# Optimization experiments

Hardware: AMD Instinct MI355X
Metric: run time of the kernel (lower is better)

Reference implementation:

```python
import jax, jax.numpy as jnp
import numpy as np

VOCAB = 256
D_MODEL = 1792
NUM_LAYERS = 4
D_STATE = 16
D_CONV = 4
EXPAND = 2
D_INNER = EXPAND * D_MODEL            # 3584
DT_RANK = (D_MODEL + 15) // 16        # 112
EPS = 1e-5


def _ln(x, w, b):
    x32 = x.astype(jnp.float32)
    mu = x32.mean(-1, keepdims=True)
    var = ((x32 - mu) ** 2).mean(-1, keepdims=True)
    return (((x32 - mu) * jax.lax.rsqrt(var + EPS)) * w + b)


def _silu(x):
    return x * jax.nn.sigmoid(x)


def _mamba_mixer(x, in_w, cw, cb, xp_w, dt_w, dt_b, A_log, Dp, out_w):
    # x: [B, L, d_model]
    B, L, _ = x.shape
    xz = jnp.einsum('bld,ed->ble', x, in_w)          # [B, L, 2*d_inner]
    xc, z = jnp.split(xz, 2, axis=-1)
    # depthwise causal conv1d over time
    xc = jax.lax.conv_general_dilated(
        xc.swapaxes(1, 2), cw[:, None, :], (1,), [(D_CONV - 1, 0)],
        feature_group_count=D_INNER,
        dimension_numbers=('NCH', 'OIH', 'NCH')).swapaxes(1, 2) + cb
    xc = _silu(xc)
    dbl = jnp.einsum('bld,ed->ble', xc, xp_w)        # [B, L, dt_rank+2*d_state]
    dt = dbl[..., :DT_RANK]
    Bm = dbl[..., DT_RANK:DT_RANK + D_STATE]
    Cm = dbl[..., DT_RANK + D_STATE:]
    dt = jax.nn.softplus(jnp.einsum('blr,dr->bld', dt, dt_w) + dt_b)  # [B,L,d_inner]
    A = -jnp.exp(A_log)                              # [d_inner, d_state]
    dA = jnp.exp(dt[..., None] * A)                  # [B, L, d_inner, d_state]
    dBx = dt[..., None] * Bm[:, :, None, :] * xc[..., None]

    def step(h, t):
        dA_t, dBx_t, C_t = t
        h = dA_t * h + dBx_t                         # [B, d_inner, d_state]
        y = jnp.einsum('bds,bs->bd', h, C_t)
        return h, y

    h0 = jnp.zeros((B, D_INNER, D_STATE), x.dtype)
    _, ys = jax.lax.scan(step, h0, (dA.swapaxes(0, 1), dBx.swapaxes(0, 1), Cm.swapaxes(0, 1)))
    y = ys.swapaxes(0, 1) + Dp * xc                  # [B, L, d_inner]
    y = y * _silu(z)
    return jnp.einsum('bld,od->blo', y, out_w)       # [B, L, d_model]


def setup_inputs() -> dict:
    key = jax.random.key(0)
    ks = jax.random.split(key, 10)
    B, L = 1, 512
    s = 0.02
    input_ids = jax.random.randint(ks[0], (B, L), 0, VOCAB, dtype=jnp.int32)
    embed = jax.random.normal(ks[1], (VOCAB, D_MODEL), jnp.float32) * s
    in_proj_w = jax.random.normal(ks[2], (NUM_LAYERS, 2 * D_INNER, D_MODEL), jnp.float32) * s
    conv_w = jax.random.normal(ks[3], (NUM_LAYERS, D_INNER, D_CONV), jnp.float32) * 0.1
    conv_b = jnp.zeros((NUM_LAYERS, D_INNER), jnp.float32)
    x_proj_w = jax.random.normal(ks[4], (NUM_LAYERS, DT_RANK + 2 * D_STATE, D_INNER), jnp.float32) * s
    dt_proj_w = jax.random.normal(ks[5], (NUM_LAYERS, D_INNER, DT_RANK), jnp.float32) * (DT_RANK ** -0.5)
    u = jax.random.uniform(ks[6], (NUM_LAYERS, D_INNER), jnp.float32)
    dt = jnp.exp(u * (jnp.log(0.1) - jnp.log(0.001)) + jnp.log(0.001))
    dt_proj_b = dt + jnp.log(-jnp.expm1(-dt))        # inverse softplus
    A_log = jnp.log(jnp.broadcast_to(jnp.arange(1, D_STATE + 1, dtype=jnp.float32), (NUM_LAYERS, D_INNER, D_STATE))) + jnp.zeros((NUM_LAYERS, D_INNER, D_STATE), jnp.float32)
    D_skip = jnp.ones((NUM_LAYERS, D_INNER), jnp.float32)
    out_proj_w = jax.random.normal(ks[7], (NUM_LAYERS, D_MODEL, D_INNER), jnp.float32) * s
    norm_w = jnp.ones((NUM_LAYERS, D_MODEL), jnp.float32)
    norm_b = jnp.zeros((NUM_LAYERS, D_MODEL), jnp.float32)
    final_norm_w = jnp.ones((D_MODEL,), jnp.float32)
    final_norm_b = jnp.zeros((D_MODEL,), jnp.float32)
    return dict(input_ids=input_ids, embed=embed, in_proj_w=in_proj_w, conv_w=conv_w,
                conv_b=conv_b, x_proj_w=x_proj_w, dt_proj_w=dt_proj_w, dt_proj_b=dt_proj_b,
                A_log=A_log, D_skip=D_skip, out_proj_w=out_proj_w, norm_w=norm_w,
                norm_b=norm_b, final_norm_w=final_norm_w, final_norm_b=final_norm_b)


def reference(input_ids, embed, in_proj_w, conv_w, conv_b, x_proj_w, dt_proj_w,
              dt_proj_b, A_log, D_skip, out_proj_w, norm_w, norm_b,
              final_norm_w, final_norm_b):
    hidden = embed[input_ids]                        # [B, L, d_model]
    residual = hidden.astype(jnp.float32)            # residual_in_fp32
    for i in range(NUM_LAYERS):
        if i > 0:
            residual = residual + hidden.astype(jnp.float32)
        h = _ln(residual, norm_w[i], norm_b[i])
        hidden = _mamba_mixer(h, in_proj_w[i], conv_w[i], conv_b[i], x_proj_w[i],
                              dt_proj_w[i], dt_proj_b[i], A_log[i], D_skip[i], out_proj_w[i])
    residual = residual + hidden.astype(jnp.float32)
    return _ln(residual, final_norm_w, final_norm_b)
```

## Files before the change

### kernel.cpp

```cpp
#include <hip/hip_runtime.h>
#include <hip/hip_bf16.h>
#include <math.h>

#define D_MODEL 1792
#define D_INNER 3584
#define D_STATE 16
#define D_CONV  4
#define DT_RANK 112
#define NLAYER  4
#define LSEQ    512
#define XPROJ_N (DT_RANK + 2 * D_STATE)
#define KSPLIT  8
#define KCHUNK  (D_INNER / KSPLIT)
#define SCH     32
#define SCL     (LSEQ / SCH)
#define INSPLIT 2
#define OUTSPLIT 4

typedef __attribute__((ext_vector_type(8))) short bf16x8;
typedef __attribute__((ext_vector_type(8))) ushort u16x8;
typedef __attribute__((ext_vector_type(4))) ushort u16x4;
typedef __attribute__((ext_vector_type(4))) float f32x4;

__device__ __forceinline__ ushort f2bf(float f) {
    unsigned u = __float_as_uint(f);
    unsigned r = (u + 0x7FFFu + ((u >> 16) & 1u)) >> 16;
    return (ushort)r;
}

__device__ __forceinline__ u16x8 cvt8(const f32x4 a, const f32x4 b) {
    u16x8 v;
    v[0] = f2bf(a[0]); v[1] = f2bf(a[1]); v[2] = f2bf(a[2]); v[3] = f2bf(a[3]);
    v[4] = f2bf(b[0]); v[5] = f2bf(b[1]); v[6] = f2bf(b[2]); v[7] = f2bf(b[3]);
    return v;
}

__global__ __launch_bounds__(256) void add_ln_kernel(float* __restrict__ res,
                                                     const float* __restrict__ hidp,
                                                     const float* __restrict__ w,
                                                     const float* __restrict__ b,
                                                     float* __restrict__ out32,
                                                     ushort* __restrict__ out16,
                                                     int mode,
                                                     const int* __restrict__ ids,
                                                     const float* __restrict__ embed) {
    const int l = blockIdx.x;
    const int t = threadIdx.x;
    __shared__ float sbuf[8];
    float loc[7];
    float* row = res + (size_t)l * D_MODEL;
    const float* erow = (mode == 2) ? (embed + (size_t)ids[l] * D_MODEL) : nullptr;

    float sum = 0.f;
#pragma unroll
    for (int i = 0; i < 7; ++i) {
        int d = t + i * 256;
        float v;
        if (mode == 2) {
            v = erow[d]; row[d] = v;
        } else {
            v = row[d];
            if (mode == 1) {
                float hv = 0.f;
#pragma unroll
                for (int z = 0; z < OUTSPLIT; ++z)
                    hv += hidp[(size_t)z * LSEQ * D_MODEL + (size_t)l * D_MODEL + d];
                v += hv; row[d] = v;
            }
        }
        loc[i] = v;
        sum += v;
    }
#pragma unroll
    for (int o = 32; o > 0; o >>= 1) sum += __shfl_down(sum, o, 64);
    if ((t & 63) == 0) sbuf[t >> 6] = sum;
    __syncthreads();
    if (t == 0) sbuf[4] = sbuf[0] + sbuf[1] + sbuf[2] + sbuf[3];
    __syncthreads();
    const float mu = sbuf[4] * (1.f / D_MODEL);

    float vs = 0.f;
#pragma unroll
    for (int i = 0; i < 7; ++i) { float d0 = loc[i] - mu; vs += d0 * d0; }
#pragma unroll
    for (int o = 32; o > 0; o >>= 1) vs += __shfl_down(vs, o, 64);
    __syncthreads();
    if ((t & 63) == 0) sbuf[t >> 6] = vs;
    __syncthreads();
    if (t == 0) sbuf[4] = sbuf[0] + sbuf[1] + sbuf[2] + sbuf[3];
    __syncthreads();
    const float rstd = rsqrtf(sbuf[4] * (1.f / D_MODEL) + 1e-5f);

#pragma unroll
    for (int i = 0; i < 7; ++i) {
        int d = t + i * 256;
        float v = (loc[i] - mu) * rstd * w[d] + b[d];
        if (out16) out16[(size_t)l * D_MODEL + d] = f2bf(v);
        else       out32[(size_t)l * D_MODEL + d] = v;
    }
}

template<int NSPLIT>
__global__ __launch_bounds__(256) void gemm128_mfma(const ushort* __restrict__ A, int lda,
                                                    const float* __restrict__ W,
                                                    float* __restrict__ C,
                                                    int N, int K) {
    constexpr int BK = 32;
    __shared__ ushort As[128 * BK];
    __shared__ ushort Bs[128 * BK];

    const int tid  = threadIdx.x;
    const int lane = tid & 63;
    const int wave = tid >> 6;
    const int m0 = blockIdx.y * 128;
    const int n0 = blockIdx.x * 128;
    const int wm = (wave >> 1) * 64;
    const int wn = (wave & 1) * 64;
    const int frow = lane & 15;
    const int fkg  = lane >> 4;
    const int kchunk = K / NSPLIT;
    const int kbase  = blockIdx.z * kchunk;
    const int M = gridDim.y * 128;

    f32x4 acc[4][4] = {};

    for (int it = 0; it < kchunk / BK; ++it) {
        const int k0 = kbase + it * BK;
#pragma unroll
        for (int i = 0; i < 2; ++i) {
            int c = tid + i * 256;
            int row = c >> 2;
            int kc  = (c & 3) * 8;
            __builtin_amdgcn_global_load_lds(
                (const __attribute__((address_space(1))) void*)(A + (size_t)(m0 + row) * lda + k0 + kc),
                (__attribute__((address_space(3))) void*)(As + c * 8), 16, 0, 0);
        }
        f32x4 w0[2], w1[2];
#pragma unroll
        for (int i = 0; i < 2; ++i) {
            int c = tid + i * 256;
            int row = c >> 2;
            int kc  = (c & 3) * 8;
            const float* p = W + (size_t)(n0 + row) * K + k0 + kc;
            w0[i] = *(const f32x4*)p;
            w1[i] = *(const f32x4*)(p + 4);
        }
#pragma unroll
        for (int i = 0; i < 2; ++i) {
            int c = tid + i * 256;
            *(u16x8*)(Bs + c * 8) = cvt8(w0[i], w1[i]);
        }
        __syncthreads();

        bf16x8 af[4];
#pragma unroll
        for (int i = 0; i < 4; ++i)
            af[i] = *(const bf16x8*)(As + (wm + i * 16 + frow) * BK + fkg * 8);

#pragma unroll
        for (int j = 0; j < 4; ++j) {
            bf16x8 bb = *(const bf16x8*)(Bs + (wn + j * 16 + frow) * BK + fkg * 8);
#pragma unroll
            for (int i = 0; i < 4; ++i)
                acc[i][j] = __builtin_amdgcn_mfma_f32_16x16x32_bf16(af[i], bb, acc[i][j], 0, 0, 0);
        }
        __syncthreads();
    }

    float* Cz = C + (size_t)blockIdx.z * M * N;
#pragma unroll
    for (int i = 0; i < 4; ++i) {
#pragma unroll
        for (int r = 0; r < 4; ++r) {
            int m = m0 + wm + i * 16 + fkg * 4 + r;
            float* cp = Cz + (size_t)m * N + n0 + wn + frow;
#pragma unroll
            for (int j = 0; j < 4; ++j)
                cp[j * 16] = acc[i][j][r];
        }
    }
}

__global__ __launch_bounds__(256) void dt_gemm(const ushort* __restrict__ A,
                                               const float* __restrict__ Wdt,
                                               float* __restrict__ C,
                                               const float* __restrict__ bias) {
    constexpr int BM = 64;
    constexpr int BK = 32;
    constexpr int N = D_INNER;
    __shared__ ushort As[BM * BK];
    __shared__ ushort Bs[128 * BK];

    const int tid  = threadIdx.x;
    const int lane = tid & 63;
    const int wave = tid >> 6;
    const int m0 = blockIdx.y * BM;
    const int n0 = blockIdx.x * 128;
    const int wm = (wave >> 1) * 32;
    const int wn = (wave & 1) * 64;
    const int frow = lane & 15;
    const int fkg  = lane >> 4;

    f32x4 acc[2][4] = {};

    for (int it = 0; it < 128 / BK; ++it) {
        const int k0 = it * BK;
        {
            int row = tid >> 2;
            int kc  = (tid & 3) * 8;
            __builtin_amdgcn_global_load_lds(
                (const __attribute__((address_space(1))) void*)(A + (size_t)(m0 + row) * 128 + k0 + kc),
                (__attribute__((address_space(3))) void*)(As + tid * 8), 16, 0, 0);
        }
        f32x4 w0[2], w1[2];
        int valid[2];
#pragma unroll
        for (int i = 0; i < 2; ++i) {
            int c = tid + i * 256;
            int row = c >> 2;
            int k   = k0 + (c & 3) * 8;
            valid[i] = (k < DT_RANK);
            const float* p = Wdt + (size_t)(n0 + row) * DT_RANK + (valid[i] ? k : 0);
            w0[i] = *(const f32x4*)p;
            w1[i] = *(const f32x4*)(p + 4);
        }
#pragma unroll
        for (int i = 0; i < 2; ++i) {
            int c = tid + i * 256;
            u16x8 v = {};
            if (valid[i]) v = cvt8(w0[i], w1[i]);
            *(u16x8*)(Bs + c * 8) = v;
        }
        __syncthreads();

        bf16x8 af[2];
#pragma unroll
        for (int i = 0; i < 2; ++i)
            af[i] = *(const bf16x8*)(As + (wm + i * 16 + frow) * BK + fkg * 8);

#pragma unroll
        for (int j = 0; j < 4; ++j) {
            bf16x8 bb = *(const bf16x8*)(Bs + (wn + j * 16 + frow) * BK + fkg * 8);
#pragma unroll
            for (int i = 0; i < 2; ++i)
                acc[i][j] = __builtin_amdgcn_mfma_f32_16x16x32_bf16(af[i], bb, acc[i][j], 0, 0, 0);
        }
        __syncthreads();
    }

    float bj[4];
#pragma unroll
    for (int j = 0; j < 4; ++j) bj[j] = bias[n0 + wn + frow + j * 16];

#pragma unroll
    for (int i = 0; i < 2; ++i) {
#pragma unroll
        for (int r = 0; r < 4; ++r) {
            int m = m0 + wm + i * 16 + fkg * 4 + r;
            float* cp = C + (size_t)m * N + n0 + wn + frow;
#pragma unroll
            for (int j = 0; j < 4; ++j) {
                float v = acc[i][j][r] + bj[j];
                v = (v > 20.f) ? v : __logf(1.f + __expf(v));
                cp[j * 16] = v;
            }
        }
    }
}

__global__ __launch_bounds__(256) void xproj_split(const ushort* __restrict__ xcbf,
                                                   const float* __restrict__ W,
                                                   float* __restrict__ xpart) {
    __shared__ ushort As[64 * 32];
    __shared__ ushort Ws[16 * 32];
    const int tid  = threadIdx.x;
    const int lane = tid & 63;
    const int wave = tid >> 6;
    const int n0 = blockIdx.x * 16;
    const int m0 = blockIdx.y * 64;
    const int z  = blockIdx.z;
    const int wm = wave * 16;
    const int frow = lane & 15;
    const int fkg  = lane >> 4;
    const int kbase = z * KCHUNK;

    f32x4 acc = {};

    for (int it = 0; it < KCHUNK / 32; ++it) {
        const int k0 = kbase + it * 32;
        {
            int row = tid >> 2;
            int kc  = (tid & 3) * 8;
            __builtin_amdgcn_global_load_lds(
                (const __attribute__((address_space(1))) void*)(xcbf + (size_t)(m0 + row) * D_INNER + k0 + kc),
                (__attribute__((address_space(3))) void*)(As + tid * 8), 16, 0, 0);
        }
        if (tid < 64) {
            int row = tid >> 2;
            int kc  = (tid & 3) * 8;
            const float* p = W + (size_t)(n0 + row) * D_INNER + k0 + kc;
            f32x4 a = *(const f32x4*)p;
            f32x4 b = *(const f32x4*)(p + 4);
            *(u16x8*)(Ws + tid * 8) = cvt8(a, b);
        }
        __syncthreads();

        bf16x8 af = *(const bf16x8*)(As + (wm + frow) * 32 + fkg * 8);
        bf16x8 bb = *(const bf16x8*)(Ws + frow * 32 + fkg * 8);
        acc = __builtin_amdgcn_mfma_f32_16x16x32_bf16(af, bb, acc, 0, 0, 0);
        __syncthreads();
    }

#pragma unroll
    for (int r = 0; r < 4; ++r) {
        int m = m0 + wm + fkg * 4 + r;
        int n = n0 + frow;
        xpart[((size_t)z * LSEQ + m) * XPROJ_N + n] = acc[r];
    }
}

__global__ __launch_bounds__(256) void xreduce_kernel(const float* __restrict__ xpart,
                                                      float* __restrict__ dbl,
                                                      ushort* __restrict__ dtb) {
    int idx = blockIdx.x * 256 + threadIdx.x;
    if (idx >= LSEQ * XPROJ_N) return;
    int m = idx / XPROJ_N;
    int n = idx - m * XPROJ_N;
    float s = 0.f;
#pragma unroll
    for (int z = 0; z < KSPLIT; ++z)
        s += xpart[(size_t)z * LSEQ * XPROJ_N + idx];
    dbl[idx] = s;
    if (n < DT_RANK)      dtb[m * 128 + n] = f2bf(s);
    else if (n < 128)     dtb[m * 128 + n] = 0;
}

__global__ __launch_bounds__(256) void conv_silu_kernel(const float* __restrict__ xzp,
                                                        const float* __restrict__ cw,
                                                        const float* __restrict__ cb,
                                                        float* __restrict__ xc,
                                                        ushort* __restrict__ xcbf) {
    const size_t SL = (size_t)LSEQ * 2 * D_INNER;
    int idx = blockIdx.x * 256 + threadIdx.x;
    if (idx >= LSEQ * D_INNER / 4) return;
    int l  = idx / (D_INNER / 4);
    int c4 = (idx - l * (D_INNER / 4)) * 4;

    const f32x4 wc0 = *(const f32x4*)(cw + (size_t)(c4 + 0) * D_CONV);
    const f32x4 wc1 = *(const f32x4*)(cw + (size_t)(c4 + 1) * D_CONV);
    const f32x4 wc2 = *(const f32x4*)(cw + (size_t)(c4 + 2) * D_CONV);
    const f32x4 wc3 = *(const f32x4*)(cw + (size_t)(c4 + 3) * D_CONV);

    f32x4 s = *(const f32x4*)(cb + c4);
#pragma unroll
    for (int k = 0; k < D_CONV; ++k) {
        int ll = l - (D_CONV - 1) + k;
        if (ll >= 0) {
            const f32x4 v0 = *(const f32x4*)(xzp + (size_t)ll * (2 * D_INNER) + c4);
            const f32x4 v1 = *(const f32x4*)(xzp + SL + (size_t)ll * (2 * D_INNER) + c4);
            s[0] = fmaf(wc0[k], v0[0] + v1[0], s[0]);
            s[1] = fmaf(wc1[k], v0[1] + v1[1], s[1]);
            s[2] = fmaf(wc2[k], v0[2] + v1[2], s[2]);
            s[3] = fmaf(wc3[k], v0[3] + v1[3], s[3]);
        }
    }
    f32x4 o;
    u16x4 ob;
#pragma unroll
    for (int q = 0; q < 4; ++q) {
        const float sig = 1.f / (1.f + __expf(-s[q]));
        o[q] = s[q] * sig;
        ob[q] = f2bf(o[q]);
    }
    *(f32x4*)(xc + (size_t)idx * 4) = o;
    *(u16x4*)(xcbf + (size_t)idx * 4) = ob;
}

__global__ __launch_bounds__(256) void scan_part1(const float* __restrict__ dt,
                                                  const float* __restrict__ xc,
                                                  const float* __restrict__ dbl,
                                                  const float* __restrict__ A_log,
                                                  float* __restrict__ P,
                                                  float* __restrict__ F) {
    const int d = blockIdx.x * 256 + threadIdx.x;
    const int c = blockIdx.y;
    __shared__ float Bs[SCL][D_STATE];
    {
        int t = threadIdx.x;
        int ll = t >> 4, s = t & 15;
        Bs[ll][s] = dbl[(size_t)(c * SCL + ll) * XPROJ_N + DT_RANK + s];
    }
    float A2[D_STATE], h[D_STATE], p[D_STATE];
#pragma unroll
    for (int s = 0; s < D_STATE; ++s) {
        A2[s] = -__expf(A_log[(size_t)d * D_STATE + s]) * 1.4426950408889634f;
        h[s] = 0.f; p[s] = 1.f;
    }
    __syncthreads();

    for (int li0 = 0; li0 < SCL; li0 += 4) {
        float dtv4[4], xcv4[4];
#pragma unroll
        for (int q = 0; q < 4; ++q) {
            const int l = c * SCL + li0 + q;
            dtv4[q] = dt[(size_t)l * D_INNER + d];
            xcv4[q] = xc[(size_t)l * D_INNER + d];
        }
#pragma unroll
        for (int q = 0; q < 4; ++q) {
            const int li = li0 + q;
            const float dtv = dtv4[q];
            const float coef = dtv * xcv4[q];
#pragma unroll
            for (int s = 0; s < D_STATE; ++s) {
                float e = exp2f(dtv * A2[s]);
                h[s] = fmaf(e, h[s], coef * Bs[li][s]);
                p[s] *= e;
            }
        }
    }
    float* Pp = P + ((size_t)c * D_INNER + d) * D_STATE;
    float* Fp = F + ((size_t)c * D_INNER + d) * D_STATE;
#pragma unroll
    for (int v = 0; v < 4; ++v) {
        *(f32x4*)(Pp + v * 4) = *(f32x4*)(p + v * 4);
        *(f32x4*)(Fp + v * 4) = *(f32x4*)(h + v * 4);
    }
}

__global__ __launch_bounds__(256) void scan_fix(const float* __restrict__ P,
                                                const float* __restrict__ F,
                                                float* __restrict__ Hin) {
    const int idx = blockIdx.x * 256 + threadIdx.x;
    if (idx >= D_INNER * D_STATE) return;
    const size_t stride = (size_t)D_INNER * D_STATE;
    float h = 0.f;
#pragma unroll
    for (int c = 0; c < SCH; ++c) {
        Hin[c * stride + idx] = h;
        h = fmaf(P[c * stride + idx], h, F[c * stride + idx]);
    }
}

__global__ __launch_bounds__(256) void scan_part3(const float* __restrict__ dt,
                                                  const float* __restrict__ xc,
                                                  const float* __restrict__ dbl,
                                                  const float* __restrict__ A_log,
                                                  const float* __restrict__ Dp,
                                                  const float* __restrict__ xzp,
                                                  const float* __restrict__ Hin,
                                                  ushort* __restrict__ ybf) {
    const size_t SL = (size_t)LSEQ * 2 * D_INNER;
    const int d = blockIdx.x * 256 + threadIdx.x;
    const int c = blockIdx.y;
    __shared__ float Bs[SCL][D_STATE];
    __shared__ float Cs[SCL][D_STATE];
    {
        int t = threadIdx.x;
        int ll = t >> 4, s = t & 15;
        Bs[ll][s] = dbl[(size_t)(c * SCL + ll) * XPROJ_N + DT_RANK + s];
        Cs[ll][s] = dbl[(size_t)(c * SCL + ll) * XPROJ_N + DT_RANK + D_STATE + s];
    }
    float A2[D_STATE], h[D_STATE];
#pragma unroll
    for (int s = 0; s < D_STATE; ++s)
        A2[s] = -__expf(A_log[(size_t)d * D_STATE + s]) * 1.4426950408889634f;
    {
        const float* Hp = Hin + ((size_t)c * D_INNER + d) * D_STATE;
#pragma unroll
        for (int v = 0; v < 4; ++v)
            *(f32x4*)(h + v * 4) = *(const f32x4*)(Hp + v * 4);
    }
    const float Dd = Dp[d];
    __syncthreads();

    for (int li0 = 0; li0 < SCL; li0 += 4) {
        float dtv4[4], xcv4[4], zv4[4];
#pragma unroll
        for (int q = 0; q < 4; ++q) {
            const int l = c * SCL + li0 + q;
            dtv4[q] = dt[(size_t)l * D_INNER + d];
            xcv4[q] = xc[(size_t)l * D_INNER + d];
            zv4[q]  = xzp[(size_t)l * (2 * D_INNER) + D_INNER + d]
                    + xzp[SL + (size_t)l * (2 * D_INNER) + D_INNER + d];
        }
#pragma unroll
        for (int q = 0; q < 4; ++q) {
            const int li = li0 + q;
            const float dtv = dtv4[q];
            const float xcv = xcv4[q];
            const float coef = dtv * xcv;
            float a0 = 0.f, a1 = 0.f, a2 = 0.f, a3 = 0.f;
#pragma unroll
            for (int s = 0; s < D_STATE; s += 4) {
                float e0 = exp2f(dtv * A2[s + 0]);
                float e1 = exp2f(dtv * A2[s + 1]);
                float e2 = exp2f(dtv * A2[s + 2]);
                float e3 = exp2f(dtv * A2[s + 3]);
                h[s + 0] = fmaf(e0, h[s + 0], coef * Bs[li][s + 0]);
                h[s + 1] = fmaf(e1, h[s + 1], coef * Bs[li][s + 1]);
                h[s + 2] = fmaf(e2, h[s + 2], coef * Bs[li][s + 2]);
                h[s + 3] = fmaf(e3, h[s + 3], coef * Bs[li][s + 3]);
                a0 = fmaf(h[s + 0], Cs[li][s + 0], a0);
                a1 = fmaf(h[s + 1], Cs[li][s + 1], a1);
                a2 = fmaf(h[s + 2], Cs[li][s + 2], a2);
                a3 = fmaf(h[s + 3], Cs[li][s + 3], a3);
            }
            const float zv = zv4[q];
            const float sig = 1.f / (1.f + __expf(-zv));
            const float y = ((a0 + a1) + (a2 + a3) + Dd * xcv) * (zv * sig);
            ybf[(size_t)(c * SCL + li) * D_INNER + d] = f2bf(y);
        }
    }
}

extern "C" void kernel_launch(void* const* d_in, const int* in_sizes, int n_in,
                              void* d_out, int out_size, void* d_ws, size_t ws_size,
                              hipStream_t stream) {
    const int*   ids       = (const int*)d_in[0];
    const float* embed     = (const float*)d_in[1];
    const float* in_proj_w = (const float*)d_in[2];
    const float* conv_w    = (const float*)d_in[3];
    const float* conv_b    = (const float*)d_in[4];
    const float* x_proj_w  = (const float*)d_in[5];
    const float* dt_proj_w = (const float*)d_in[6];
    const float* dt_proj_b = (const float*)d_in[7];
    const float* A_log     = (const float*)d_in[8];
    const float* D_skip    = (const float*)d_in[9];
    const float* out_proj_w= (const float*)d_in[10];
    const float* norm_w    = (const float*)d_in[11];
    const float* norm_b    = (const float*)d_in[12];
    const float* fin_w     = (const float*)d_in[13];
    const float* fin_b     = (const float*)d_in[14];
    float* out = (float*)d_out;

    float* ws = (float*)d_ws;
    float* res    = ws; ws += LSEQ * D_MODEL;
    float* xzp    = ws; ws += (size_t)INSPLIT * LSEQ * 2 * D_INNER;
    float* xc     = ws; ws += (size_t)LSEQ * D_INNER;
    float* dbl    = ws; ws += LSEQ * XPROJ_N;
    float* dty    = ws; ws += (size_t)LSEQ * D_INNER;
    float* xpart  = ws; ws += (size_t)KSPLIT * LSEQ * XPROJ_N;
    float* Pbuf   = ws; ws += (size_t)SCH * D_INNER * D_STATE;
    float* Fbuf   = ws; ws += (size_t)SCH * D_INNER * D_STATE;
    float* HinB   = ws; ws += (size_t)SCH * D_INNER * D_STATE;
    ushort* hbf   = (ushort*)ws; ws += (LSEQ * D_MODEL) / 2;
    ushort* ybf   = (ushort*)ws; ws += (LSEQ * D_INNER) / 2;
    ushort* xcbf  = (ushort*)ws; ws += (LSEQ * D_INNER) / 2;
    ushort* dtb   = (ushort*)ws; ws += (LSEQ * 128) / 2;
    float* outp = Pbuf;

    for (int i = 0; i < NLAYER; ++i) {
        add_ln_kernel<<<LSEQ, 256, 0, stream>>>(
            res, outp, norm_w + (size_t)i * D_MODEL, norm_b + (size_t)i * D_MODEL,
            nullptr, hbf, i > 0 ? 1 : 2, ids, embed);

        gemm128_mfma<INSPLIT><<<dim3(2 * D_INNER / 128, LSEQ / 128, INSPLIT), 256, 0, stream>>>(
            hbf, D_MODEL, in_proj_w + (size_t)i * 2 * D_INNER * D_MODEL, xzp,
            2 * D_INNER, D_MODEL);

        conv_silu_kernel<<<(LSEQ * D_INNER / 4 + 255) / 256, 256, 0, stream>>>(
            xzp, conv_w + (size_t)i * D_INNER * D_CONV, conv_b + (size_t)i * D_INNER,
            xc, xcbf);

        xproj_split<<<dim3(XPROJ_N / 16, LSEQ / 64, KSPLIT), 256, 0, stream>>>(
            xcbf, x_proj_w + (size_t)i * XPROJ_N * D_INNER, xpart);
        xreduce_kernel<<<(LSEQ * XPROJ_N + 255) / 256, 256, 0, stream>>>(xpart, dbl, dtb);

        dt_gemm<<<dim3(D_INNER / 128, LSEQ / 64, 1), 256, 0, stream>>>(
            dtb, dt_proj_w + (size_t)i * D_INNER * DT_RANK, dty,
            dt_proj_b + (size_t)i * D_INNER);

        scan_part1<<<dim3(D_INNER / 256, SCH), 256, 0, stream>>>(
            dty, xc, dbl, A_log + (size_t)i * D_INNER * D_STATE, Pbuf, Fbuf);
        scan_fix<<<(D_INNER * D_STATE + 255) / 256, 256, 0, stream>>>(Pbuf, Fbuf, HinB);
        scan_part3<<<dim3(D_INNER / 256, SCH), 256, 0, stream>>>(
            dty, xc, dbl, A_log + (size_t)i * D_INNER * D_STATE,
            D_skip + (size_t)i * D_INNER, xzp, HinB, ybf);

        gemm128_mfma<OUTSPLIT><<<dim3(D_MODEL / 128, LSEQ / 128, OUTSPLIT), 256, 0, stream>>>(
            ybf, D_INNER, out_proj_w + (size_t)i * D_MODEL * D_INNER, outp,
            D_MODEL, D_INNER);
    }

    add_ln_kernel<<<LSEQ, 256, 0, stream>>>(res, outp, fin_w, fin_b, out, nullptr, 1,
                                            nullptr, nullptr);
}
```

Measured before the change: 1.007 ms.

## Double-buffer LDS tiles in MFMA GEMM and raise out-proj split-K

Adds double-buffered shared-memory tiles to the bf16 MFMA GEMM so the global loads for the next K-tile are issued before the MFMAs on the current tile. The fp32 weights are converted and stored into the other buffer after the compute, which leaves one barrier per iteration. This is meant to hide global load latency behind the matrix math. Separately, the out-projection split-K factor goes from 4 to 8, with its partial buffer moved to a dedicated workspace region because Pbuf can no longer hold it. This adds parallelism at the cost of doubled LDS use, more partial-sum traffic and a larger reduction, and it depends on the workspace being big enough.

```diff
diff --git a/kernel.cpp b/kernel.cpp
--- a/kernel.cpp
+++ b/kernel.cpp
@@ -15,7 +15,7 @@
 #define SCH     32
 #define SCL     (LSEQ / SCH)
 #define INSPLIT 2
-#define OUTSPLIT 4
+#define OUTSPLIT 8
 
 typedef __attribute__((ext_vector_type(8))) short bf16x8;
 typedef __attribute__((ext_vector_type(8))) ushort u16x8;
@@ -106,8 +106,8 @@
                                                     float* __restrict__ C,
                                                     int N, int K) {
     constexpr int BK = 32;
-    __shared__ ushort As[128 * BK];
-    __shared__ ushort Bs[128 * BK];
+    __shared__ ushort As[2][128 * BK];
+    __shared__ ushort Bs[2][128 * BK];
 
     const int tid  = threadIdx.x;
     const int lane = tid & 63;
@@ -121,48 +121,66 @@
     const int kchunk = K / NSPLIT;
     const int kbase  = blockIdx.z * kchunk;
     const int M = gridDim.y * 128;
+    const int nIter = kchunk / BK;
+
+    const int r0 = tid >> 2;
+    const int r1 = r0 + 64;
+    const int kc = (tid & 3) * 8;
 
     f32x4 acc[4][4] = {};
-
-    for (int it = 0; it < kchunk / BK; ++it) {
-        const int k0 = kbase + it * BK;
-#pragma unroll
-        for (int i = 0; i < 2; ++i) {
-            int c = tid + i * 256;
-            int row = c >> 2;
-            int kc  = (c & 3) * 8;
+    f32x4 wa0, wa1, wb0, wb1;
+
+    {
+        __builtin_amdgcn_global_load_lds(
+            (const __attribute__((address_space(1))) void*)(A + (size_t)(m0 + r0) * lda + kbase + kc),
+            (__attribute__((address_space(3))) void*)(&As[0][tid * 8]), 16, 0, 0);
+        __builtin_amdgcn_global_load_lds(
+            (const __attribute__((address_space(1))) void*)(A + (size_t)(m0 + r1) * lda + kbase + kc),
+            (__attribute__((address_space(3))) void*)(&As[0][(tid + 256) * 8]), 16, 0, 0);
+        const float* p0 = W + (size_t)(n0 + r0) * K + kbase + kc;
+        const float* p1 = W + (size_t)(n0 + r1) * K + kbase + kc;
+        wa0 = *(const f32x4*)p0; wa1 = *(const f32x4*)(p0 + 4);
+        wb0 = *(const f32x4*)p1; wb1 = *(const f32x4*)(p1 + 4);
+        *(u16x8*)(&Bs[0][tid * 8]) = cvt8(wa0, wa1);
+        *(u16x8*)(&Bs[0][(tid + 256) * 8]) = cvt8(wb0, wb1);
+    }
+    __syncthreads();
+
+    for (int it = 0; it < nIter; ++it) {
+        const int cur = it & 1;
+        const int nxt = cur ^ 1;
+        const bool hasNext = (it + 1) < nIter;
+
+        if (hasNext) {
+            const int k0 = kbase + (it + 1) * BK;
             __builtin_amdgcn_global_load_lds(
-                (const __attribute__((address_space(1))) void*)(A + (size_t)(m0 + row) * lda + k0 + kc),
-                (__attribute__((address_space(3))) void*)(As + c * 8), 16, 0, 0);
-        }
-        f32x4 w0[2], w1[2];
-#pragma unroll
-        for (int i = 0; i < 2; ++i) {
-            int c = tid + i * 256;
-            int row = c >> 2;
-            int kc  = (c & 3) * 8;
-            const float* p = W + (size_t)(n0 + row) * K + k0 + kc;
-            w0[i] = *(const f32x4*)p;
-            w1[i] = *(const f32x4*)(p + 4);
-        }
-#pragma unroll
-        for (int i = 0; i < 2; ++i) {
-            int c = tid + i * 256;
-            *(u16x8*)(Bs + c * 8) = cvt8(w0[i], w1[i]);
-        }
-        __syncthreads();
+                (const __attribute__((address_space(1))) void*)(A + (size_t)(m0 + r0) * lda + k0 + kc),
+                (__attribute__((address_space(3))) void*)(&As[nxt][tid * 8]), 16, 0, 0);
+            __builtin_amdgcn_global_load_lds(
+                (const __attribute__((address_space(1))) void*)(A + (size_t)(m0 + r1) * lda + k0 + kc),
+                (__attribute__((address_space(3))) void*)(&As[nxt][(tid + 256) * 8]), 16, 0, 0);
+            const float* p0 = W + (size_t)(n0 + r0) * K + k0 + kc;
+            const float* p1 = W + (size_t)(n0 + r1) * K + k0 + kc;
+            wa0 = *(const f32x4*)p0; wa1 = *(const f32x4*)(p0 + 4);
+            wb0 = *(const f32x4*)p1; wb1 = *(const f32x4*)(p1 + 4);
+        }
 
         bf16x8 af[4];
 #pragma unroll
         for (int i = 0; i < 4; ++i)
-            af[i] = *(const bf16x8*)(As + (wm + i * 16 + frow) * BK + fkg * 8);
+            af[i] = *(const bf16x8*)(&As[cur][(wm + i * 16 + frow) * BK + fkg * 8]);
 
 #pragma unroll
         for (int j = 0; j < 4; ++j) {
-            bf16x8 bb = *(const bf16x8*)(Bs + (wn + j * 16 + frow) * BK + fkg * 8);
+            bf16x8 bb = *(const bf16x8*)(&Bs[cur][(wn + j * 16 + frow) * BK + fkg * 8]);
 #pragma unroll
             for (int i = 0; i < 4; ++i)
                 acc[i][j] = __builtin_amdgcn_mfma_f32_16x16x32_bf16(af[i], bb, acc[i][j], 0, 0, 0);
+        }
+
+        if (hasNext) {
+            *(u16x8*)(&Bs[nxt][tid * 8]) = cvt8(wa0, wa1);
+            *(u16x8*)(&Bs[nxt][(tid + 256) * 8]) = cvt8(wb0, wb1);
         }
         __syncthreads();
     }
@@ -207,9 +225,9 @@
         const int k0 = it * BK;
         {
             int row = tid >> 2;
-            int kc  = (tid & 3) * 8;
+            int kcA = (tid & 3) * 8;
             __builtin_amdgcn_global_load_lds(
-                (const __attribute__((address_space(1))) void*)(A + (size_t)(m0 + row) * 128 + k0 + kc),
+                (const __attribute__((address_space(1))) void*)(A + (size_t)(m0 + row) * 128 + k0 + kcA),
                 (__attribute__((address_space(3))) void*)(As + tid * 8), 16, 0, 0);
         }
         f32x4 w0[2], w1[2];
@@ -544,11 +562,11 @@
     float* Pbuf   = ws; ws += (size_t)SCH * D_INNER * D_STATE;
     float* Fbuf   = ws; ws += (size_t)SCH * D_INNER * D_STATE;
     float* HinB   = ws; ws += (size_t)SCH * D_INNER * D_STATE;
+    float* outp   = ws; ws += (size_t)OUTSPLIT * LSEQ * D_MODEL;
     ushort* hbf   = (ushort*)ws; ws += (LSEQ * D_MODEL) / 2;
     ushort* ybf   = (ushort*)ws; ws += (LSEQ * D_INNER) / 2;
     ushort* xcbf  = (ushort*)ws; ws += (LSEQ * D_INNER) / 2;
     ushort* dtb   = (ushort*)ws; ws += (LSEQ * 128) / 2;
-    float* outp = Pbuf;
 
     for (int i = 0; i < NLAYER; ++i) {
         add_ln_kernel<<<LSEQ, 256, 0, stream>>>(
```

New measurement: 933.2 us. 7.4% less time.
